# Optimization experiments

Hardware: AMD Instinct MI355X
Metric: run time of the kernel (lower is better)

The kernel has to match this reference:

```python
import jax, jax.numpy as jnp
import numpy as np

FP8_MAX = 448.0  # max finite value of float8_e4m3fn


def _fp8_quant_dequant(t, scale):
    """Per-tensor static FP8 e4m3fn quantize -> dequantize (simulated real quant)."""
    q = jnp.clip(t / scale, -FP8_MAX, FP8_MAX).astype(jnp.float8_e4m3fn)
    return q.astype(jnp.float32) * scale


def setup_inputs() -> dict:
    key = jax.random.key(0)
    k1, k2, k3 = jax.random.split(key, 3)
    M, K, N = 4096, 4096, 14336  # tokens, in_features, out_features
    x = jax.random.normal(k1, (M, K), jnp.float32)
    weight = jax.random.normal(k2, (N, K), jnp.float32) * 0.02
    bias = jax.random.normal(k3, (N,), jnp.float32) * 0.01
    # static per-tensor calibration scales (amax / fp8_max)
    input_scale = (jnp.max(jnp.abs(x)) / FP8_MAX).reshape(1)
    weight_scale = (jnp.max(jnp.abs(weight)) / FP8_MAX).reshape(1)
    return {"x": x, "weight": weight, "bias": bias,
            "input_scale": input_scale, "weight_scale": weight_scale}


def reference(x, weight, bias, input_scale, weight_scale):
    # QParamsLinear forward: statically quantize input to fp8 e4m3fn with the
    # input quantizer's per-tensor scale, dequantize the fp8 weight with its
    # per-tensor scale, run the GEMM (y = x_dq @ W_dq^T), and add bias.
    s_in = input_scale[0]
    s_w = weight_scale[0]
    x_dq = _fp8_quant_dequant(x, s_in)      # [M, K]
    w_dq = _fp8_quant_dequant(weight, s_w)  # [N, K]
    return jnp.einsum('mk,nk->mn', x_dq, w_dq) + bias[None, :]
```

## Files before the change

kernel.cpp:

```cpp
#include <hip/hip_runtime.h>
#include <stdint.h>

typedef float f32x4 __attribute__((ext_vector_type(4)));
typedef int   i32x8 __attribute__((ext_vector_type(8)));
typedef long  i64x2 __attribute__((ext_vector_type(2)));

#define FP8_MAX_V 448.0f

__device__ __forceinline__ uint32_t pack4_fp8(float a, float b, float c, float d) {
    a = fminf(fmaxf(a, -FP8_MAX_V), FP8_MAX_V);
    b = fminf(fmaxf(b, -FP8_MAX_V), FP8_MAX_V);
    c = fminf(fmaxf(c, -FP8_MAX_V), FP8_MAX_V);
    d = fminf(fmaxf(d, -FP8_MAX_V), FP8_MAX_V);
    int v = 0;
    v = __builtin_amdgcn_cvt_pk_fp8_f32(a, b, v, false);
    v = __builtin_amdgcn_cvt_pk_fp8_f32(c, d, v, true);
    return (uint32_t)v;
}

__global__ void quant_fp8_kernel(const float* __restrict__ in,
                                 uint32_t* __restrict__ out,
                                 const float* __restrict__ scale_ptr,
                                 long long n4) {
    const float s = scale_ptr[0];
    long long i = (long long)blockIdx.x * blockDim.x + threadIdx.x;
    const long long stride = (long long)gridDim.x * blockDim.x;
    const float4* in4 = (const float4*)in;
    for (; i < n4; i += stride) {
        float4 v = in4[i];
        out[i] = pack4_fp8(v.x / s, v.y / s, v.z / s, v.w / s);
    }
}

__global__ __launch_bounds__(256, 2) void gemm_mxfp8_kernel(
    const uint8_t* __restrict__ qA,
    const uint8_t* __restrict__ qB,
    const float* __restrict__ bias,
    const float* __restrict__ s_in_p,
    const float* __restrict__ s_w_p,
    float* __restrict__ C,
    int M, int N, int K) {
    __shared__ uint8_t lds[2][32768];

    const int tid = threadIdx.x;
    const int w   = tid >> 6;
    const int l   = tid & 63;
    const int wr  = w >> 1;
    const int wc  = w & 1;
    const int lr  = l & 15;
    const int lg  = l >> 4;
    const int lsw = lr & 7;

    const int cpx = (int)gridDim.x >> 3;
    const int swz = ((int)blockIdx.x & 7) * cpx + ((int)blockIdx.x >> 3);
    const int bm  = (swz & 15) << 8;
    const int bn  = (swz >> 4) << 7;

    const float outscale = s_in_p[0] * s_w_p[0];
    const int NT = K >> 7;

    const int off0 = (((lg << 1) ^ lsw) << 4);
    const int off1 = off0 ^ 16;

    f32x4 acc[8][4];
#pragma unroll
    for (int mi = 0; mi < 8; ++mi)
#pragma unroll
        for (int ni = 0; ni < 4; ++ni)
            acc[mi][ni] = (f32x4){0.f, 0.f, 0.f, 0.f};

    const int srow = tid >> 3;
    const int sc   = (((tid & 7) ^ (srow & 7)) << 4);
    const uint8_t* sA = qA + (size_t)(bm + srow) * K + sc;
    const int dstw = w << 10;

    const uint8_t* bR0 = qB + (size_t)(bn + wc * 64 +  0 + lr) * K + (lg << 5);
    const uint8_t* bR1 = qB + (size_t)(bn + wc * 64 + 16 + lr) * K + (lg << 5);
    const uint8_t* bR2 = qB + (size_t)(bn + wc * 64 + 32 + lr) * K + (lg << 5);
    const uint8_t* bR3 = qB + (size_t)(bn + wc * 64 + 48 + lr) * K + (lg << 5);

    union frag { i32x8 v; i64x2 h[2]; };
    frag pb0[4], pb1[4];

#define STAGE_A(SL, KB) do { \
    _Pragma("unroll") \
    for (int i = 0; i < 8; ++i) { \
        __builtin_amdgcn_global_load_lds( \
            (const __attribute__((address_space(1))) void*)(sA + (size_t)(i * 32) * K + (KB)), \
            (__attribute__((address_space(3))) void*)(&lds[SL][0] + i * 4096 + dstw), 16, 0, 0); \
    } } while (0)

#define LOAD_B(BUF, KB) do { \
    BUF[0].h[0] = *(const i64x2*)(bR0 + (KB));      BUF[0].h[1] = *(const i64x2*)(bR0 + (KB) + 16); \
    BUF[1].h[0] = *(const i64x2*)(bR1 + (KB));      BUF[1].h[1] = *(const i64x2*)(bR1 + (KB) + 16); \
    BUF[2].h[0] = *(const i64x2*)(bR2 + (KB));      BUF[2].h[1] = *(const i64x2*)(bR2 + (KB) + 16); \
    BUF[3].h[0] = *(const i64x2*)(bR3 + (KB));      BUF[3].h[1] = *(const i64x2*)(bR3 + (KB) + 16); \
} while (0)

#define TILE_BODY(TT, SLOT, BCUR, BNXT) do { \
    const int tn = ((TT) + 1 < NT) ? (TT) + 1 : 0; \
    STAGE_A((SLOT) ^ 1, tn << 7); \
    __builtin_amdgcn_sched_barrier(0); \
    LOAD_B(BNXT, (size_t)tn << 7); \
    __builtin_amdgcn_sched_barrier(0); \
    const uint8_t* sbase = &lds[SLOT][0]; \
    _Pragma("unroll") \
    for (int mi = 0; mi < 8; ++mi) { \
        frag ua; \
        const uint8_t* p = sbase + ((wr * 128 + mi * 16 + lr) << 7); \
        ua.h[0] = *(const i64x2*)(p + off0); \
        ua.h[1] = *(const i64x2*)(p + off1); \
        _Pragma("unroll") \
        for (int ni = 0; ni < 4; ++ni) \
            acc[mi][ni] = __builtin_amdgcn_mfma_scale_f32_16x16x128_f8f6f4( \
                ua.v, BCUR[ni].v, acc[mi][ni], 0, 0, 0, 127, 0, 127); \
    } \
    asm volatile("s_waitcnt lgkmcnt(0)" ::: "memory"); \
    __builtin_amdgcn_sched_barrier(0); \
    asm volatile("s_waitcnt vmcnt(8)" ::: "memory"); \
    __builtin_amdgcn_s_barrier(); \
} while (0)

    STAGE_A(0, 0);
    LOAD_B(pb0, 0);
    asm volatile("s_waitcnt vmcnt(0)" ::: "memory");
    __builtin_amdgcn_s_barrier();

    for (int T = 0; T < NT; T += 2) {
        TILE_BODY(T,     0, pb0, pb1);
        TILE_BODY(T + 1, 1, pb1, pb0);
    }

    const int crow0 = bm + wr * 128 + (lg << 2);
    const int ccol0 = bn + wc * 64 + lr;
#pragma unroll
    for (int ni = 0; ni < 4; ++ni) {
        const int col = ccol0 + ni * 16;
        const float bv = bias[col];
#pragma unroll
        for (int mi = 0; mi < 8; ++mi) {
            const int row = crow0 + mi * 16;
#pragma unroll
            for (int r = 0; r < 4; ++r)
                C[(size_t)(row + r) * N + col] = acc[mi][ni][r] * outscale + bv;
        }
    }
#undef STAGE_A
#undef LOAD_B
#undef TILE_BODY
}

extern "C" void kernel_launch(void* const* d_in, const int* in_sizes, int n_in,
                              void* d_out, int out_size, void* d_ws, size_t ws_size,
                              hipStream_t stream) {
    const float* x    = (const float*)d_in[0];
    const float* wt   = (const float*)d_in[1];
    const float* bias = (const float*)d_in[2];
    const float* s_in = (const float*)d_in[3];
    const float* s_w  = (const float*)d_in[4];
    float* out = (float*)d_out;

    const long long xe = in_sizes[0];
    const long long we = in_sizes[1];
    const int N = in_sizes[2];
    const int K = (int)(we / N);
    const int M = (int)(xe / K);

    uint8_t* qx = (uint8_t*)d_ws;
    uint8_t* qw = qx + xe;

    quant_fp8_kernel<<<2048, 256, 0, stream>>>(x,  (uint32_t*)qx, s_in, xe >> 2);
    quant_fp8_kernel<<<2048, 256, 0, stream>>>(wt, (uint32_t*)qw, s_w,  we >> 2);

    dim3 grid((M / 256) * (N / 128));
    gemm_mxfp8_kernel<<<grid, 256, 0, stream>>>(qx, qw, bias, s_in, s_w, out,
                                                M, N, K);
}
```

Before: 442.1 us.

## Pre-pack FP8 weights into MFMA fragment tiles and use 8-wave GEMM blocks

The weight quantization kernel now writes FP8 values in a 16x128 tiled layout that matches the MFMA B-operand fragment. Each lane can then fetch its 32-byte fragment with one contiguous load instead of two strided row loads. The GEMM moves to 512 threads per block, so each wave owns a 64x64 sub-tile with half the accumulators, which reduces register pressure. It also batches the LDS A-fragment reads before the MFMA burst, raises wave priority around the MFMAs, and waits only for A loads at the end of each tile. The weight quant kernel now does scattered 4-byte writes and extra index arithmetic, and the larger block adds barrier cost across 8 waves.

```diff
diff --git a/kernel.cpp b/kernel.cpp
--- a/kernel.cpp
+++ b/kernel.cpp
@@ -32,9 +32,28 @@
     }
 }
 
-__global__ __launch_bounds__(256, 2) void gemm_mxfp8_kernel(
+__global__ void quant_pack_kernel(const float* __restrict__ in,
+                                  uint8_t* __restrict__ out,
+                                  const float* __restrict__ scale_ptr,
+                                  uint32_t total4, int K4, int KT) {
+    const float s = scale_ptr[0];
+    uint32_t i = blockIdx.x * blockDim.x + threadIdx.x;
+    const uint32_t stride = gridDim.x * blockDim.x;
+    const float4* in4 = (const float4*)in;
+    for (; i < total4; i += stride) {
+        const int m  = i / K4;
+        const int k0 = (i - (uint32_t)m * K4) << 2;
+        float4 v = in4[i];
+        const uint32_t q = pack4_fp8(v.x / s, v.y / s, v.z / s, v.w / s);
+        const size_t addr = ((size_t)(m >> 4) * KT + (k0 >> 7)) * 2048
+                          + (((k0 >> 5) & 3) << 9) + ((m & 15) << 5) + (k0 & 31);
+        *(uint32_t*)(out + addr) = q;
+    }
+}
+
+__global__ __launch_bounds__(512, 2) void gemm_hy_kernel(
     const uint8_t* __restrict__ qA,
-    const uint8_t* __restrict__ qB,
+    const uint8_t* __restrict__ pB,
     const float* __restrict__ bias,
     const float* __restrict__ s_in_p,
     const float* __restrict__ s_w_p,
@@ -58,13 +77,14 @@
 
     const float outscale = s_in_p[0] * s_w_p[0];
     const int NT = K >> 7;
+    const int KT = NT;
 
     const int off0 = (((lg << 1) ^ lsw) << 4);
     const int off1 = off0 ^ 16;
 
-    f32x4 acc[8][4];
-#pragma unroll
-    for (int mi = 0; mi < 8; ++mi)
+    f32x4 acc[4][4];
+#pragma unroll
+    for (int mi = 0; mi < 4; ++mi)
 #pragma unroll
         for (int ni = 0; ni < 4; ++ni)
             acc[mi][ni] = (f32x4){0.f, 0.f, 0.f, 0.f};
@@ -74,71 +94,70 @@
     const uint8_t* sA = qA + (size_t)(bm + srow) * K + sc;
     const int dstw = w << 10;
 
-    const uint8_t* bR0 = qB + (size_t)(bn + wc * 64 +  0 + lr) * K + (lg << 5);
-    const uint8_t* bR1 = qB + (size_t)(bn + wc * 64 + 16 + lr) * K + (lg << 5);
-    const uint8_t* bR2 = qB + (size_t)(bn + wc * 64 + 32 + lr) * K + (lg << 5);
-    const uint8_t* bR3 = qB + (size_t)(bn + wc * 64 + 48 + lr) * K + (lg << 5);
+    const uint8_t* bBase = pB + ((size_t)((bn >> 4) + wc * 4) * KT) * 2048 + l * 32;
 
     union frag { i32x8 v; i64x2 h[2]; };
-    frag pb0[4], pb1[4];
+    frag b0[4], b1[4];
 
 #define STAGE_A(SL, KB) do { \
     _Pragma("unroll") \
-    for (int i = 0; i < 8; ++i) { \
+    for (int i = 0; i < 4; ++i) { \
         __builtin_amdgcn_global_load_lds( \
-            (const __attribute__((address_space(1))) void*)(sA + (size_t)(i * 32) * K + (KB)), \
-            (__attribute__((address_space(3))) void*)(&lds[SL][0] + i * 4096 + dstw), 16, 0, 0); \
+            (const __attribute__((address_space(1))) void*)(sA + (size_t)(i * 64) * K + (KB)), \
+            (__attribute__((address_space(3))) void*)(&lds[SL][0] + i * 8192 + dstw), 16, 0, 0); \
     } } while (0)
 
-#define LOAD_B(BUF, KB) do { \
-    BUF[0].h[0] = *(const i64x2*)(bR0 + (KB));      BUF[0].h[1] = *(const i64x2*)(bR0 + (KB) + 16); \
-    BUF[1].h[0] = *(const i64x2*)(bR1 + (KB));      BUF[1].h[1] = *(const i64x2*)(bR1 + (KB) + 16); \
-    BUF[2].h[0] = *(const i64x2*)(bR2 + (KB));      BUF[2].h[1] = *(const i64x2*)(bR2 + (KB) + 16); \
-    BUF[3].h[0] = *(const i64x2*)(bR3 + (KB));      BUF[3].h[1] = *(const i64x2*)(bR3 + (KB) + 16); \
+#define LOAD_B(BUF, KTI) do { \
+    _Pragma("unroll") \
+    for (int q = 0; q < 4; ++q) \
+        BUF[q].v = *(const i32x8*)(bBase + ((size_t)q * KT + (KTI)) * 2048); \
 } while (0)
 
 #define TILE_BODY(TT, SLOT, BCUR, BNXT) do { \
     const int tn = ((TT) + 1 < NT) ? (TT) + 1 : 0; \
-    STAGE_A((SLOT) ^ 1, tn << 7); \
-    __builtin_amdgcn_sched_barrier(0); \
-    LOAD_B(BNXT, (size_t)tn << 7); \
+    STAGE_A((SLOT) ^ 1, (size_t)tn << 7); \
+    LOAD_B(BNXT, tn); \
     __builtin_amdgcn_sched_barrier(0); \
     const uint8_t* sbase = &lds[SLOT][0]; \
-    _Pragma("unroll") \
-    for (int mi = 0; mi < 8; ++mi) { \
-        frag ua; \
-        const uint8_t* p = sbase + ((wr * 128 + mi * 16 + lr) << 7); \
-        ua.h[0] = *(const i64x2*)(p + off0); \
-        ua.h[1] = *(const i64x2*)(p + off1); \
+    frag ua[4]; \
+    _Pragma("unroll") \
+    for (int mi = 0; mi < 4; ++mi) { \
+        const uint8_t* p = sbase + ((wr * 64 + mi * 16 + lr) << 7); \
+        ua[mi].h[0] = *(const i64x2*)(p + off0); \
+        ua[mi].h[1] = *(const i64x2*)(p + off1); \
+    } \
+    asm volatile("s_waitcnt lgkmcnt(0)" ::: "memory"); \
+    __builtin_amdgcn_sched_barrier(0); \
+    __builtin_amdgcn_s_setprio(1); \
+    _Pragma("unroll") \
+    for (int mi = 0; mi < 4; ++mi) \
         _Pragma("unroll") \
         for (int ni = 0; ni < 4; ++ni) \
             acc[mi][ni] = __builtin_amdgcn_mfma_scale_f32_16x16x128_f8f6f4( \
-                ua.v, BCUR[ni].v, acc[mi][ni], 0, 0, 0, 127, 0, 127); \
-    } \
-    asm volatile("s_waitcnt lgkmcnt(0)" ::: "memory"); \
-    __builtin_amdgcn_sched_barrier(0); \
-    asm volatile("s_waitcnt vmcnt(8)" ::: "memory"); \
+                ua[mi].v, BCUR[ni].v, acc[mi][ni], 0, 0, 0, 127, 0, 127); \
+    __builtin_amdgcn_s_setprio(0); \
+    asm volatile("s_waitcnt vmcnt(4)" ::: "memory"); \
     __builtin_amdgcn_s_barrier(); \
 } while (0)
 
     STAGE_A(0, 0);
-    LOAD_B(pb0, 0);
-    asm volatile("s_waitcnt vmcnt(0)" ::: "memory");
+    LOAD_B(b0, 0);
+    asm volatile("s_waitcnt vmcnt(4)" ::: "memory");
     __builtin_amdgcn_s_barrier();
 
     for (int T = 0; T < NT; T += 2) {
-        TILE_BODY(T,     0, pb0, pb1);
-        TILE_BODY(T + 1, 1, pb1, pb0);
-    }
-
-    const int crow0 = bm + wr * 128 + (lg << 2);
+        TILE_BODY(T,     0, b0, b1);
+        TILE_BODY(T + 1, 1, b1, b0);
+    }
+
+    const int crow0 = bm + wr * 64 + (lg << 2);
     const int ccol0 = bn + wc * 64 + lr;
 #pragma unroll
     for (int ni = 0; ni < 4; ++ni) {
         const int col = ccol0 + ni * 16;
         const float bv = bias[col];
 #pragma unroll
-        for (int mi = 0; mi < 8; ++mi) {
+        for (int mi = 0; mi < 4; ++mi) {
             const int row = crow0 + mi * 16;
 #pragma unroll
             for (int r = 0; r < 4; ++r)
@@ -165,14 +184,17 @@
     const int N = in_sizes[2];
     const int K = (int)(we / N);
     const int M = (int)(xe / K);
+    const int K4 = K >> 2;
+    const int KT = K >> 7;
 
     uint8_t* qx = (uint8_t*)d_ws;
     uint8_t* qw = qx + xe;
 
-    quant_fp8_kernel<<<2048, 256, 0, stream>>>(x,  (uint32_t*)qx, s_in, xe >> 2);
-    quant_fp8_kernel<<<2048, 256, 0, stream>>>(wt, (uint32_t*)qw, s_w,  we >> 2);
+    quant_fp8_kernel<<<2048, 256, 0, stream>>>(x, (uint32_t*)qx, s_in, xe >> 2);
+    quant_pack_kernel<<<2048, 256, 0, stream>>>(wt, qw, s_w,
+                                                (uint32_t)(we >> 2), K4, KT);
 
     dim3 grid((M / 256) * (N / 128));
-    gemm_mxfp8_kernel<<<grid, 256, 0, stream>>>(qx, qw, bias, s_in, s_w, out,
-                                                M, N, K);
-}
+    gemm_hy_kernel<<<grid, 512, 0, stream>>>(qx, qw, bias, s_in, s_w, out,
+                                             M, N, K);
+}
```

Result: slower. 463.0 us (+4.7%).
